# Optimization experiments

Measured on AMD Instinct MI355X. Metric: run time of the kernel, lower is better.

The kernel has to match this reference:

```python
import jax, jax.numpy as jnp
import numpy as np

B, L, H, NB, D, DH = 8, 4096, 16, 8, 1024, 128

def setup_inputs() -> dict:
    key = jax.random.key(0)
    ks = jax.random.split(key, 12)
    theta_path = jax.random.normal(ks[0], (B, L, H, NB), jnp.float32)
    content_emb = jax.random.normal(ks[1], (B, L, D), jnp.float32)
    s_in = 1.0 / np.sqrt(D).astype(np.float32)
    s_h = 1.0 / np.sqrt(DH).astype(np.float32)
    # log_R_head: Linear(D,128) -> GELU -> Linear(128, H*NB), last layer weight *0.01, bias 0
    r_w1 = jax.random.normal(ks[2], (D, DH), jnp.float32) * s_in
    r_b1 = jnp.zeros((DH,), jnp.float32)
    r_w2 = jax.random.normal(ks[3], (DH, H * NB), jnp.float32) * s_h * 0.01
    r_b2 = jnp.zeros((H * NB,), jnp.float32)
    # measure_head
    m_w1 = jax.random.normal(ks[4], (D, DH), jnp.float32) * s_in
    m_b1 = jax.random.normal(ks[5], (DH,), jnp.float32) * s_in
    m_w2 = jax.random.normal(ks[6], (DH, H * NB), jnp.float32) * s_h
    m_b2 = jax.random.normal(ks[7], (H * NB,), jnp.float32) * s_h
    log_Q = jnp.full((H, NB), -3.0, jnp.float32)
    log_R_avg = jnp.full((H, NB), 1.0, jnp.float32)
    return {"theta_path": theta_path, "content_emb": content_emb,
            "log_Q": log_Q, "log_R_avg": log_R_avg,
            "r_w1": r_w1, "r_b1": r_b1, "r_w2": r_w2, "r_b2": r_b2,
            "m_w1": m_w1, "m_b1": m_b1, "m_w2": m_w2, "m_b2": m_b2}

def _mlp(x, w1, b1, w2, b2):
    h = jax.nn.gelu(x @ w1 + b1, approximate=False)  # torch nn.GELU default = exact
    return h @ w2 + b2

def reference(theta_path, content_emb, log_Q, log_R_avg,
              r_w1, r_b1, r_w2, r_b2, m_w1, m_b1, m_w2, m_b2):
    b, l, h, nb = theta_path.shape
    log_R = jnp.clip(_mlp(content_emb, r_w1, r_b1, r_w2, r_b2).reshape(b, l, h, nb), -5.0, 5.0)
    R = jnp.exp(log_R)
    z = jnp.pi * jnp.tanh(_mlp(content_emb, m_w1, m_b1, m_w2, m_b2).reshape(b, l, h, nb))
    diff = z - theta_path
    nu = jnp.arctan2(jnp.sin(diff), jnp.cos(diff))  # wrap angle error to (-pi, pi]
    Q = jnp.exp(log_Q)
    Ravg = jnp.exp(log_R_avg)
    Pi_dare = 0.5 * (-Q + jnp.sqrt(Q * Q + 4.0 * Q * Ravg))  # [H, NB]
    Pi = jnp.broadcast_to(Pi_dare[None, None], (b, l, h, nb))
    K = Pi / jnp.maximum(Pi + R, 1e-8)
    alpha = 1.0 - K
    u = K * nu
    # affine associative scan over sequence dim: d_t = alpha_t * d_{t-1} + u_t
    def combine(c1, c2):
        a1, u1 = c1
        a2, u2 = c2
        return (a2 * a1, a2 * u1 + u2)
    _, d = jax.lax.associative_scan(combine, (alpha, u), axis=1)
    return (theta_path + d, Pi, K, R)
```

## Files before the change

kernel.cpp:

```cpp
#include <hip/hip_runtime.h>
#include <hip/hip_bf16.h>
#include <cstdint>
#include <cstddef>

#define TOK 32768
#define CCH 128
#define DIN 1024

typedef __attribute__((ext_vector_type(8))) short short8;
typedef __attribute__((ext_vector_type(4))) float f32x4;

#define LIST_CAP 262144u

static __device__ __forceinline__ uint16_t f2bf(float f) {
  __hip_bfloat16 h = __float2bfloat16(f);
  return __builtin_bit_cast(uint16_t, h);
}
static __device__ __forceinline__ float bf2f(uint16_t u) {
  __hip_bfloat16 h = __builtin_bit_cast(__hip_bfloat16, u);
  return __bfloat162float(h);
}
static __device__ __forceinline__ void splitbf(float x, uint16_t& hi, uint16_t& lo) {
  hi = f2bf(x);
  lo = f2bf(x - bf2f(hi));
}

__global__ void prep_kernel(const float* __restrict__ r_w1, const float* __restrict__ r_w2,
                            const float* __restrict__ m_w1, const float* __restrict__ m_w2,
                            const float* __restrict__ logQ, const float* __restrict__ logRavg,
                            uint16_t* __restrict__ W1r, uint16_t* __restrict__ W2r,
                            uint16_t* __restrict__ W1mh, uint16_t* __restrict__ W1ml,
                            uint16_t* __restrict__ W2mh, uint16_t* __restrict__ W2ml,
                            float* __restrict__ PiArr, unsigned int* __restrict__ cnt)
{
  int idx = blockIdx.x * 256 + threadIdx.x;
  if (idx == 0) cnt[0] = 0;
  if (idx < 131072) {
    int e = idx;
    int j = e & 7, lane = (e >> 3) & 63, nt = (e >> 9) & 7, c = (e >> 12) & 1, kt = e >> 13;
    int k = kt * 64 + c * 32 + (lane >> 4) * 8 + j;
    int n = nt * 16 + (lane & 15);
    W1r[e] = f2bf(r_w1[k * 128 + n]);
  } else if (idx < 147456) {
    int e = idx - 131072;
    int j = e & 7, l = (e >> 3) & 63, c = (e >> 9) & 3, t = e >> 11;
    int k = c * 32 + (l >> 4) * 8 + j;
    int col = t * 16 + (l & 15);
    W2r[e] = f2bf(r_w2[k * 128 + col]);
  } else if (idx < 278528) {
    int e = idx - 147456;
    int j = e & 7, lane = (e >> 3) & 63, nt = (e >> 9) & 7, c = (e >> 12) & 1, kt = e >> 13;
    int k = kt * 64 + c * 32 + (lane >> 4) * 8 + j;
    int n = nt * 16 + (lane & 15);
    uint16_t h, l;
    splitbf(m_w1[k * 128 + n], h, l);
    W1mh[e] = h; W1ml[e] = l;
  } else if (idx < 294912) {
    int e = idx - 278528;
    int j = e & 7, l = (e >> 3) & 63, c = (e >> 9) & 3, t = e >> 11;
    int k = c * 32 + (l >> 4) * 8 + j;
    int col = t * 16 + (l & 15);
    uint16_t h, lo;
    splitbf(m_w2[k * 128 + col], h, lo);
    W2mh[e] = h; W2ml[e] = lo;
  } else if (idx < 295040) {
    int i = idx - 294912;
    float Q = expf(logQ[i]);
    float Rv = expf(logRavg[i]);
    PiArr[i] = 0.5f * (-Q + sqrtf(Q * Q + 4.0f * Q * Rv));
  }
}

__global__ __launch_bounds__(512, 4) void fused_all(
    const float* __restrict__ X, const float* __restrict__ theta,
    const uint16_t* __restrict__ W1r, const uint16_t* __restrict__ W2r,
    const uint16_t* __restrict__ W1h, const uint16_t* __restrict__ W1l,
    const uint16_t* __restrict__ W2h, const uint16_t* __restrict__ W2l,
    const float* __restrict__ rB1, const float* __restrict__ rB2,
    const float* __restrict__ B1, const float* __restrict__ B2,
    const float* __restrict__ PiArr,
    float* __restrict__ out0, float* __restrict__ out1,
    float* __restrict__ out2, float* __restrict__ out3,
    float* __restrict__ AggA, float* __restrict__ AggU,
    unsigned int* __restrict__ cnt, unsigned int* __restrict__ list)
{
  union SM {
    struct { uint16_t Xh[2][64][72]; uint16_t Xl[2][64][72]; } s1;
    struct { uint16_t Hh[64][136]; uint16_t Hl[64][136]; uint16_t Hr[64][136]; } s2;
    struct { float2 Agg[4][4][128]; } s3;
  };
  __shared__ SM sm;

  const int tid = threadIdx.x;
  const int w = tid >> 6, lane = tid & 63;
  const int l15 = lane & 15, l4 = lane >> 4;
  const int tn = w;
  const int tok0 = blockIdx.x * 64;

  f32x4 accm[4], accr[4];
#pragma unroll
  for (int m = 0; m < 4; ++m) { accm[m] = 0.0f; accr[m] = 0.0f; }

  const int rr = tid >> 4, cc = tid & 15;
  float4 xa0, xa1;

  auto ldX = [&](int kt, float4& v0, float4& v1) {
    v0 = *reinterpret_cast<const float4*>(
        X + (size_t)(tok0 + rr) * DIN + kt * 64 + cc * 4);
    v1 = *reinterpret_cast<const float4*>(
        X + (size_t)(tok0 + rr + 32) * DIN + kt * 64 + cc * 4);
  };
  auto wrX = [&](int b, const float4& v0, const float4& v1) {
    ushort4 vh, vl;
    splitbf(v0.x, vh.x, vl.x);
    splitbf(v0.y, vh.y, vl.y);
    splitbf(v0.z, vh.z, vl.z);
    splitbf(v0.w, vh.w, vl.w);
    *reinterpret_cast<ushort4*>(&sm.s1.Xh[b][rr][cc * 4]) = vh;
    *reinterpret_cast<ushort4*>(&sm.s1.Xl[b][rr][cc * 4]) = vl;
    splitbf(v1.x, vh.x, vl.x);
    splitbf(v1.y, vh.y, vl.y);
    splitbf(v1.z, vh.z, vl.z);
    splitbf(v1.w, vh.w, vl.w);
    *reinterpret_cast<ushort4*>(&sm.s1.Xh[b][rr + 32][cc * 4]) = vh;
    *reinterpret_cast<ushort4*>(&sm.s1.Xl[b][rr + 32][cc * 4]) = vl;
  };
  auto ldB = [&](int kt, short8 (&h)[2], short8 (&l)[2], short8 (&r)[2]) {
#pragma unroll
    for (int c = 0; c < 2; ++c) {
      const size_t boff = (size_t)((((kt * 2 + c) * 8 + tn) * 64 + lane) * 8);
      h[c] = *reinterpret_cast<const short8*>(W1h + boff);
      l[c] = *reinterpret_cast<const short8*>(W1l + boff);
      r[c] = *reinterpret_cast<const short8*>(W1r + boff);
    }
  };

  short8 bhc[2], blc[2], brc[2], bhn[2], bln[2], brn[2];
  ldX(0, xa0, xa1);
  wrX(0, xa0, xa1);
  ldB(0, bhc, blc, brc);
  __syncthreads();

#pragma unroll
  for (int kt = 0; kt < 16; ++kt) {
    const int cur = kt & 1;

    if (kt < 15) {
      ldX(kt + 1, xa0, xa1);
      ldB(kt + 1, bhn, bln, brn);
    }

#pragma unroll
    for (int c = 0; c < 2; ++c) {
      const int ko = c * 32 + l4 * 8;
#pragma unroll
      for (int m = 0; m < 4; ++m) {
        const int row = m * 16 + l15;
        const short8 ah = *reinterpret_cast<const short8*>(&sm.s1.Xh[cur][row][ko]);
        const short8 al = *reinterpret_cast<const short8*>(&sm.s1.Xl[cur][row][ko]);
        accm[m] = __builtin_amdgcn_mfma_f32_16x16x32_bf16(ah, bhc[c], accm[m], 0, 0, 0);
        accm[m] = __builtin_amdgcn_mfma_f32_16x16x32_bf16(al, bhc[c], accm[m], 0, 0, 0);
        accm[m] = __builtin_amdgcn_mfma_f32_16x16x32_bf16(ah, blc[c], accm[m], 0, 0, 0);
        accr[m] = __builtin_amdgcn_mfma_f32_16x16x32_bf16(ah, brc[c], accr[m], 0, 0, 0);
      }
    }

    if (kt < 15) wrX(cur ^ 1, xa0, xa1);

    asm volatile("s_waitcnt lgkmcnt(0)" ::: "memory");
    __builtin_amdgcn_s_barrier();

#pragma unroll
    for (int c = 0; c < 2; ++c) { bhc[c] = bhn[c]; blc[c] = bln[c]; brc[c] = brn[c]; }
  }

  short8 b2h[4], b2l[4], b2r[4];
#pragma unroll
  for (int c2 = 0; c2 < 4; ++c2) {
    const size_t boff = (size_t)(((tn * 4 + c2) * 64 + lane) * 8);
    b2h[c2] = *reinterpret_cast<const short8*>(W2h + boff);
    b2l[c2] = *reinterpret_cast<const short8*>(W2l + boff);
    b2r[c2] = *reinterpret_cast<const short8*>(W2r + boff);
  }

  const int n = tn * 16 + l15;
  {
    const float b1m = B1[n];
    const float b1rr = rB1[n];
#pragma unroll
    for (int m = 0; m < 4; ++m)
#pragma unroll
      for (int r = 0; r < 4; ++r) {
        const int row = m * 16 + l4 * 4 + r;
        const float v = accm[m][r] + b1m;
        const float ev = erff(v / 1.41421356237309515f);
        const float g = 0.5f * v * (ev + 1.0f);
        uint16_t gh, gl;
        splitbf(g, gh, gl);
        sm.s2.Hh[row][n] = gh;
        sm.s2.Hl[row][n] = gl;
        const float vr = accr[m][r] + b1rr;
        const float gr = 0.5f * vr * (1.0f + erff(vr * 0.70710678118654752f));
        sm.s2.Hr[row][n] = f2bf(gr);
      }
  }
  __syncthreads();

  f32x4 acc2m[4], acc2r[4];
#pragma unroll
  for (int m = 0; m < 4; ++m) { acc2m[m] = 0.0f; acc2r[m] = 0.0f; }

#pragma unroll
  for (int c2 = 0; c2 < 4; ++c2) {
    const int ko = c2 * 32 + l4 * 8;
#pragma unroll
    for (int m = 0; m < 4; ++m) {
      const int row = m * 16 + l15;
      const short8 ah = *reinterpret_cast<const short8*>(&sm.s2.Hh[row][ko]);
      const short8 al = *reinterpret_cast<const short8*>(&sm.s2.Hl[row][ko]);
      const short8 ar = *reinterpret_cast<const short8*>(&sm.s2.Hr[row][ko]);
      acc2m[m] = __builtin_amdgcn_mfma_f32_16x16x32_bf16(ah, b2h[c2], acc2m[m], 0, 0, 0);
      acc2m[m] = __builtin_amdgcn_mfma_f32_16x16x32_bf16(al, b2h[c2], acc2m[m], 0, 0, 0);
      acc2m[m] = __builtin_amdgcn_mfma_f32_16x16x32_bf16(ah, b2l[c2], acc2m[m], 0, 0, 0);
      acc2r[m] = __builtin_amdgcn_mfma_f32_16x16x32_bf16(ar, b2r[c2], acc2r[m], 0, 0, 0);
    }
  }

  {
    const float b2 = rB2[n];
    const float piv = PiArr[n];
#pragma unroll
    for (int m = 0; m < 4; ++m)
#pragma unroll
      for (int r = 0; r < 4; ++r) {
        const int token = tok0 + m * 16 + l4 * 4 + r;
        float lr = acc2r[m][r] + b2;
        lr = fminf(fmaxf(lr, -5.0f), 5.0f);
        const float R = expf(lr);
        const float K = piv / fmaxf(piv + R, 1e-8f);
        const size_t off = (size_t)token * CCH + n;
        out1[off] = piv;
        out2[off] = K;
        out3[off] = R;
        acc2r[m][r] = K;
      }
  }

  {
    const float b2 = B2[n];
#pragma unroll
    for (int m = 0; m < 4; ++m)
#pragma unroll
      for (int r = 0; r < 4; ++r) {
        const int token = tok0 + m * 16 + l4 * 4 + r;
        const float mz = acc2m[m][r] + b2;
        const float z = 3.14159265358979323846f * tanhf(mz);
        const float d = z - theta[(size_t)token * CCH + n];
        const float wr = d - 6.2831853071795864769f * rintf(d * 0.15915494309189533577f);
        if (3.14159265358979323846f - fabsf(wr) < 3e-4f) {
          unsigned int p = atomicAdd(cnt, 1u);
          if (p < LIST_CAP) list[p] = (unsigned int)(token * CCH + n);
        }
        out0[(size_t)token * CCH + n] = wr;
        acc2m[m][r] = wr;
      }
  }

  __syncthreads();
#pragma unroll
  for (int m = 0; m < 4; ++m) {
    float A = 1.0f, U = 0.0f;
#pragma unroll
    for (int r = 0; r < 4; ++r) {
      const float k = acc2r[m][r];
      const float v = acc2m[m][r];
      const float a = 1.0f - k;
      A *= a;
      U = fmaf(a, U, k * v);
    }
    sm.s3.Agg[m][l4][n] = make_float2(A, U);
  }
  __syncthreads();
  if (tid < 128) {
    const int ch = tid;
    float A = 1.0f, U = 0.0f;
#pragma unroll
    for (int g = 0; g < 16; ++g) {
      const float2 au = sm.s3.Agg[g >> 2][g & 3][ch];
      U = fmaf(au.x, U, au.y);
      A *= au.x;
    }
    AggA[blockIdx.x * CCH + ch] = A;
    AggU[blockIdx.x * CCH + ch] = U;
  }
}

__global__ __launch_bounds__(128) void refine_nu(
    const float* __restrict__ X, const float* __restrict__ theta,
    const float* __restrict__ W1, const float* __restrict__ B1,
    const float* __restrict__ W2, const float* __restrict__ B2,
    const unsigned int* __restrict__ cnt, const unsigned int* __restrict__ list,
    float* __restrict__ out0)
{
  __shared__ float h[128];
  const int j = threadIdx.x;
  const unsigned int n = min(cnt[0], LIST_CAP);
  for (unsigned int e = blockIdx.x; e < n; e += gridDim.x) {
    const unsigned int idx = list[e];
    const int tok = (int)(idx >> 7), ch = (int)(idx & 127);
    const float* xr = X + (size_t)tok * DIN;
    float acc = 0.0f;
    for (int k = 0; k < DIN; ++k)
      acc = fmaf(xr[k], W1[(size_t)k * CCH + j], acc);
    const float v = acc + B1[j];
    const float ev = erff(v / 1.41421356237309515f);
    h[j] = 0.5f * v * (ev + 1.0f);
    __syncthreads();
    if (j == 0) {
      float a2 = 0.0f;
      for (int k = 0; k < CCH; ++k)
        a2 = fmaf(h[k], W2[(size_t)k * CCH + ch], a2);
      const float mz = a2 + B2[ch];
      const float z = 3.14159265358979323846f * tanhf(mz);
      const float d = z - theta[(size_t)tok * CCH + ch];
      out0[(size_t)tok * CCH + ch] = atan2f(sinf(d), cosf(d));
    }
    __syncthreads();
  }
}

__global__ __launch_bounds__(64) void refine_agg(
    const float* __restrict__ Kk, const float* __restrict__ nu,
    const unsigned int* __restrict__ cnt, const unsigned int* __restrict__ list,
    float* __restrict__ AggA, float* __restrict__ AggU)
{
  __shared__ float av[64], uv[64];
  const int i = threadIdx.x;
  const unsigned int n = min(cnt[0], LIST_CAP);
  for (unsigned int e = blockIdx.x; e < n; e += gridDim.x) {
    const unsigned int idx = list[e];
    const int ch = (int)(idx & 127);
    const int blk = (int)(idx >> 13);
    const size_t off = (size_t)(blk * 64 + i) * CCH + ch;
    const float k = Kk[off];
    const float v = nu[off];
    av[i] = 1.0f - k;
    uv[i] = k * v;
    __syncthreads();
    if (i == 0) {
      float A = 1.0f, U = 0.0f;
      for (int g = 0; g < 64; ++g) {
        U = fmaf(av[g], U, uv[g]);
        A *= av[g];
      }
      AggA[blk * CCH + ch] = A;
      AggU[blk * CCH + ch] = U;
    }
    __syncthreads();
  }
}

__global__ __launch_bounds__(256) void scan_pass2(
    const float* __restrict__ AggA, const float* __restrict__ AggU,
    float* __restrict__ Carry)
{
  const int wid = blockIdx.x * 4 + (threadIdx.x >> 6);
  const int b = wid >> 7, ch = wid & 127;
  const int g = threadIdx.x & 63;
  const size_t idx = (size_t)(b * 64 + g) * CCH + ch;
  float A = AggA[idx];
  float U = AggU[idx];
#pragma unroll
  for (int s = 1; s < 64; s <<= 1) {
    const float pA = __shfl_up(A, s);
    const float pU = __shfl_up(U, s);
    if (g >= s) {
      U = fmaf(A, pU, U);
      A = A * pA;
    }
  }
  float cU = __shfl_up(U, 1);
  if (g == 0) cU = 0.0f;
  Carry[idx] = cU;
}

__global__ __launch_bounds__(128) void scan_pass3(
    const float* __restrict__ Kk, const float* __restrict__ theta,
    const float* __restrict__ Carry, float* __restrict__ out0)
{
  __shared__ float kb[64 * CCH];
  __shared__ float vb[64 * CCH];
  const int c = threadIdx.x;
  const int blk = blockIdx.x;
  const size_t base = (size_t)blk * 64 * CCH;
#pragma unroll
  for (int i = 0; i < 16; ++i) {
    const int e = i * 128 + c;
    reinterpret_cast<float4*>(kb)[e] = reinterpret_cast<const float4*>(Kk + base)[e];
    reinterpret_cast<float4*>(vb)[e] = reinterpret_cast<const float4*>(out0 + base)[e];
  }
  __syncthreads();
  float d = Carry[blk * CCH + c];
#pragma unroll 8
  for (int i = 0; i < 64; ++i) {
    const float k = kb[i * CCH + c];
    const float v = vb[i * CCH + c];
    d = fmaf(1.0f - k, d, k * v);
    const size_t off = base + (size_t)i * CCH + c;
    out0[off] = theta[off] + d;
  }
}

extern "C" void kernel_launch(void* const* d_in, const int* in_sizes, int n_in,
                              void* d_out, int out_size, void* d_ws, size_t ws_size,
                              hipStream_t stream) {
  const float* theta   = (const float*)d_in[0];
  const float* X       = (const float*)d_in[1];
  const float* logQ    = (const float*)d_in[2];
  const float* logRavg = (const float*)d_in[3];
  const float* r_w1    = (const float*)d_in[4];
  const float* r_b1    = (const float*)d_in[5];
  const float* r_w2    = (const float*)d_in[6];
  const float* r_b2    = (const float*)d_in[7];
  const float* m_w1    = (const float*)d_in[8];
  const float* m_b1    = (const float*)d_in[9];
  const float* m_w2    = (const float*)d_in[10];
  const float* m_b2    = (const float*)d_in[11];

  float* out0 = (float*)d_out;
  float* out1 = out0 + 4194304;
  float* out2 = out0 + 2 * 4194304;
  float* out3 = out0 + 3 * 4194304;

  char* ws = (char*)d_ws;
  uint16_t* W1r  = (uint16_t*)(ws);
  uint16_t* W2r  = (uint16_t*)(ws + 262144);
  float* PiArr   = (float*)(ws + 295936);
  float* AggA    = (float*)(ws + 296448);
  float* AggU    = (float*)(ws + 558592);
  float* Carry   = (float*)(ws + 820736);
  unsigned int* cnt  = (unsigned int*)(ws + 1082880);
  unsigned int* list = (unsigned int*)(ws + 1083136);
  uint16_t* W1mh = (uint16_t*)(ws + 2131712);
  uint16_t* W1ml = (uint16_t*)(ws + 2393856);
  uint16_t* W2mh = (uint16_t*)(ws + 2656000);
  uint16_t* W2ml = (uint16_t*)(ws + 2688768);

  prep_kernel<<<1153, 256, 0, stream>>>(r_w1, r_w2, m_w1, m_w2, logQ, logRavg,
                                        W1r, W2r, W1mh, W1ml, W2mh, W2ml,
                                        PiArr, cnt);
  fused_all<<<512, 512, 0, stream>>>(X, theta, W1r, W2r, W1mh, W1ml, W2mh, W2ml,
                                     r_b1, r_b2, m_b1, m_b2, PiArr,
                                     out0, out1, out2, out3, AggA, AggU, cnt, list);
  refine_nu<<<1024, 128, 0, stream>>>(X, theta, m_w1, m_b1, m_w2, m_b2,
                                      cnt, list, out0);
  refine_agg<<<1024, 64, 0, stream>>>(out2, out0, cnt, list, AggA, AggU);
  scan_pass2<<<256, 256, 0, stream>>>(AggA, AggU, Carry);
  scan_pass3<<<512, 128, 0, stream>>>(out2, theta, Carry, out0);
}
```

Baseline: 122.8 us.

## Deepen X prefetch to two stages and split K-tile MFMA phases with priority

The global load of X now runs two tiles ahead, holding an extra register pair, instead of one. Each K-tile's MFMA work is split into two halves separated by an extra barrier. Shared-memory A fragments are batched before each half, and the loads are spread across the halves: X in the first, W1 in the second. s_setprio raises wave priority around the MFMA bursts to encourage compute/memory interleaving across waves, at the cost of an extra barrier per iteration and higher register pressure.

After: 127.4 us. 3.8% more time.

```diff
diff --git a/kernel.cpp b/kernel.cpp
--- a/kernel.cpp
+++ b/kernel.cpp
@@ -102,7 +102,7 @@
   for (int m = 0; m < 4; ++m) { accm[m] = 0.0f; accr[m] = 0.0f; }
 
   const int rr = tid >> 4, cc = tid & 15;
-  float4 xa0, xa1;
+  float4 xa0, xa1, xb0, xb1;
 
   auto ldX = [&](int kt, float4& v0, float4& v1) {
     v0 = *reinterpret_cast<const float4*>(
@@ -138,6 +138,7 @@
   short8 bhc[2], blc[2], brc[2], bhn[2], bln[2], brn[2];
   ldX(0, xa0, xa1);
   wrX(0, xa0, xa1);
+  ldX(1, xa0, xa1);
   ldB(0, bhc, blc, brc);
   __syncthreads();
 
@@ -145,28 +146,50 @@
   for (int kt = 0; kt < 16; ++kt) {
     const int cur = kt & 1;
 
-    if (kt < 15) {
-      ldX(kt + 1, xa0, xa1);
-      ldB(kt + 1, bhn, bln, brn);
-    }
-
-#pragma unroll
-    for (int c = 0; c < 2; ++c) {
-      const int ko = c * 32 + l4 * 8;
+    {
+      short8 ah[4], al[4];
+      const int ko = l4 * 8;
 #pragma unroll
       for (int m = 0; m < 4; ++m) {
         const int row = m * 16 + l15;
-        const short8 ah = *reinterpret_cast<const short8*>(&sm.s1.Xh[cur][row][ko]);
-        const short8 al = *reinterpret_cast<const short8*>(&sm.s1.Xl[cur][row][ko]);
-        accm[m] = __builtin_amdgcn_mfma_f32_16x16x32_bf16(ah, bhc[c], accm[m], 0, 0, 0);
-        accm[m] = __builtin_amdgcn_mfma_f32_16x16x32_bf16(al, bhc[c], accm[m], 0, 0, 0);
-        accm[m] = __builtin_amdgcn_mfma_f32_16x16x32_bf16(ah, blc[c], accm[m], 0, 0, 0);
-        accr[m] = __builtin_amdgcn_mfma_f32_16x16x32_bf16(ah, brc[c], accr[m], 0, 0, 0);
-      }
-    }
-
-    if (kt < 15) wrX(cur ^ 1, xa0, xa1);
-
+        ah[m] = *reinterpret_cast<const short8*>(&sm.s1.Xh[cur][row][ko]);
+        al[m] = *reinterpret_cast<const short8*>(&sm.s1.Xl[cur][row][ko]);
+      }
+      if (kt < 14) ldX(kt + 2, xb0, xb1);
+      __builtin_amdgcn_s_setprio(1);
+#pragma unroll
+      for (int m = 0; m < 4; ++m) {
+        accm[m] = __builtin_amdgcn_mfma_f32_16x16x32_bf16(ah[m], bhc[0], accm[m], 0, 0, 0);
+        accm[m] = __builtin_amdgcn_mfma_f32_16x16x32_bf16(al[m], bhc[0], accm[m], 0, 0, 0);
+        accm[m] = __builtin_amdgcn_mfma_f32_16x16x32_bf16(ah[m], blc[0], accm[m], 0, 0, 0);
+        accr[m] = __builtin_amdgcn_mfma_f32_16x16x32_bf16(ah[m], brc[0], accr[m], 0, 0, 0);
+      }
+      __builtin_amdgcn_s_setprio(0);
+    }
+    asm volatile("s_waitcnt lgkmcnt(0)" ::: "memory");
+    __builtin_amdgcn_s_barrier();
+
+    {
+      short8 ah[4], al[4];
+      const int ko = 32 + l4 * 8;
+#pragma unroll
+      for (int m = 0; m < 4; ++m) {
+        const int row = m * 16 + l15;
+        ah[m] = *reinterpret_cast<const short8*>(&sm.s1.Xh[cur][row][ko]);
+        al[m] = *reinterpret_cast<const short8*>(&sm.s1.Xl[cur][row][ko]);
+      }
+      if (kt < 15) ldB(kt + 1, bhn, bln, brn);
+      __builtin_amdgcn_s_setprio(1);
+#pragma unroll
+      for (int m = 0; m < 4; ++m) {
+        accm[m] = __builtin_amdgcn_mfma_f32_16x16x32_bf16(ah[m], bhc[1], accm[m], 0, 0, 0);
+        accm[m] = __builtin_amdgcn_mfma_f32_16x16x32_bf16(al[m], bhc[1], accm[m], 0, 0, 0);
+        accm[m] = __builtin_amdgcn_mfma_f32_16x16x32_bf16(ah[m], blc[1], accm[m], 0, 0, 0);
+        accr[m] = __builtin_amdgcn_mfma_f32_16x16x32_bf16(ah[m], brc[1], accr[m], 0, 0, 0);
+      }
+      __builtin_amdgcn_s_setprio(0);
+    }
+    if (kt < 15) { wrX(cur ^ 1, xa0, xa1); xa0 = xb0; xa1 = xb1; }
     asm volatile("s_waitcnt lgkmcnt(0)" ::: "memory");
     __builtin_amdgcn_s_barrier();
 
```
